# Kernel tuning notes

Hardware: AMD Instinct MI355X
Metric: run time of the kernel (lower is better)

Reference implementation:

```python
import jax, jax.numpy as jnp
import numpy as np

HEAD_DIM = 256
NUM_HEADS = 8
NUM_KV_HEADS = 1
ROPE_BASE = 10000.0
NEG_INF = -1e9


def _rope_cos_sin(position_ids):
    # inv_freq: [head_dim/2]
    inv_freq = 1.0 / (ROPE_BASE ** (jnp.arange(0, HEAD_DIM, 2, dtype=jnp.float32) / HEAD_DIM))
    # freqs: [B, S, head_dim/2]
    freqs = position_ids.astype(jnp.float32)[:, :, None] * inv_freq[None, None, :]
    emb = jnp.concatenate([freqs, freqs], axis=-1)  # [B, S, head_dim]
    return jnp.cos(emb), jnp.sin(emb)


def _rotate_half(x):
    x1, x2 = x[..., : HEAD_DIM // 2], x[..., HEAD_DIM // 2 :]
    return jnp.concatenate([-x2, x1], axis=-1)


def setup_inputs() -> dict:
    key = jax.random.key(0)
    ks = jax.random.split(key, 5)
    B, S, D = 2, 2048, 2048
    hidden_states = jax.random.normal(ks[0], (B, S, D), dtype=jnp.float32)
    # additive causal mask: 0 on/below diagonal, -1e9 above
    causal = jnp.triu(jnp.full((S, S), NEG_INF, dtype=jnp.float32), k=1)
    attention_mask = jnp.broadcast_to(causal[None, None], (B, 1, S, S))
    position_ids = jnp.broadcast_to(jnp.arange(S, dtype=jnp.int64 if jax.config.jax_enable_x64 else jnp.int32)[None], (B, S))
    Wq = jax.random.normal(ks[1], (NUM_HEADS * HEAD_DIM, D), dtype=jnp.float32) * 0.02
    Wk = jax.random.normal(ks[2], (NUM_KV_HEADS * HEAD_DIM, D), dtype=jnp.float32) * 0.02
    Wv = jax.random.normal(ks[3], (NUM_KV_HEADS * HEAD_DIM, D), dtype=jnp.float32) * 0.02
    Wo = jax.random.normal(ks[4], (D, NUM_HEADS * HEAD_DIM), dtype=jnp.float32) * 0.02
    return {"hidden_states": hidden_states, "attention_mask": attention_mask,
            "position_ids": position_ids, "Wq": Wq, "Wk": Wk, "Wv": Wv, "Wo": Wo}


def reference(hidden_states, attention_mask, position_ids, Wq, Wk, Wv, Wo):
    B, S, D = hidden_states.shape
    n_rep = NUM_HEADS // NUM_KV_HEADS
    # projections (no bias)
    q = (hidden_states @ Wq.T).reshape(B, S, NUM_HEADS, HEAD_DIM).transpose(0, 2, 1, 3)
    k = (hidden_states @ Wk.T).reshape(B, S, NUM_KV_HEADS, HEAD_DIM).transpose(0, 2, 1, 3)
    v = (hidden_states @ Wv.T).reshape(B, S, NUM_KV_HEADS, HEAD_DIM).transpose(0, 2, 1, 3)
    # rotary embeddings, broadcast over heads (unsqueeze_dim=1)
    cos, sin = _rope_cos_sin(position_ids)  # [B, S, head_dim]
    cos, sin = cos[:, None], sin[:, None]
    q = q * cos + _rotate_half(q) * sin
    k = k * cos + _rotate_half(k) * sin
    # repeat_kv: expand kv heads to match query heads
    k = jnp.repeat(k, n_rep, axis=1)  # [B, H, S, Dh]
    v = jnp.repeat(v, n_rep, axis=1)
    scores = jnp.einsum('bhqd,bhkd->bhqk', q, k) / jnp.sqrt(jnp.float32(HEAD_DIM))
    scores = scores + attention_mask
    attn_weights = jax.nn.softmax(scores.astype(jnp.float32), axis=-1).astype(q.dtype)
    attn_output = jnp.einsum('bhqk,bhkd->bhqd', attn_weights, v)
    attn_output = attn_output.transpose(0, 2, 1, 3).reshape(B, S, NUM_HEADS * HEAD_DIM)
    attn_output = attn_output @ Wo.T
    return attn_output, attn_weights
```

## Files before the change

### kernel.cpp

```cpp
#include <hip/hip_runtime.h>
#include <math.h>

#define SEQ 2048
#define DM  2048
#define NH  8
#define HD  256
#define NB  2

typedef __attribute__((ext_vector_type(8))) short bf16x8;
typedef __attribute__((ext_vector_type(4))) float f32x4;

__device__ inline short f2b(float f) {
    union { float f; unsigned u; } x; x.f = f;
    unsigned r = x.u + 0x7fffu + ((x.u >> 16) & 1u);
    return (short)(r >> 16);
}
__device__ inline float b2f(short s) {
    union { unsigned u; float f; } x;
    x.u = ((unsigned)(unsigned short)s) << 16;
    return x.f;
}

typedef unsigned int u32_g __attribute__((address_space(1)));
typedef unsigned int u32_l __attribute__((address_space(3)));
__device__ inline void gl2lds(const void* g, void* l) {
    __builtin_amdgcn_global_load_lds((const u32_g*)g, (u32_l*)l, 16, 0, 0);
}

__global__ void convert_all(const float* __restrict__ hs, const float* __restrict__ wq,
                            const float* __restrict__ wk, const float* __restrict__ wv,
                            const float* __restrict__ wo,
                            short* __restrict__ hsb, short* __restrict__ wcat,
                            short* __restrict__ wob)
{
    int i4 = blockIdx.x * 256 + threadIdx.x;
    const float* src; short* dst; int s4, d4;
    if (i4 < 2097152)      { src = hs; dst = hsb;  s4 = i4;           d4 = s4; }
    else if (i4 < 3145728) { src = wq; dst = wcat; s4 = i4 - 2097152; d4 = s4; }
    else if (i4 < 3276800) { src = wk; dst = wcat; s4 = i4 - 3145728; d4 = 1048576 + s4; }
    else if (i4 < 3407872) { src = wv; dst = wcat; s4 = i4 - 3276800; d4 = 1179648 + s4; }
    else                   { src = wo; dst = wob;  s4 = i4 - 3407872; d4 = s4; }
    float4 v = ((const float4*)src)[s4];
    short4 o;
    o.x = f2b(v.x); o.y = f2b(v.y); o.z = f2b(v.z); o.w = f2b(v.w);
    ((short4*)dst)[d4] = o;
}

template<int MODE>
__global__ __launch_bounds__(256, 2) void gemm_bt(const short* __restrict__ A,
                                                  const short* __restrict__ Bw,
                                                  float* __restrict__ C,
                                                  short* __restrict__ q_o,
                                                  short* __restrict__ k_o,
                                                  short* __restrict__ v_o,
                                                  int M, int N, int K)
{
    __shared__ short As[128 * 32];
    __shared__ short Bs[128 * 32];
    int tid = threadIdx.x;
    int lane = tid & 63, w = tid >> 6;
    int lm = lane & 15, quad = lane >> 4;
    int wm = w & 1, wn = w >> 1;
    int m0 = blockIdx.y * 128, n0 = blockIdx.x * 128;

    f32x4 acc[16];
#pragma unroll
    for (int i = 0; i < 16; ++i) acc[i] = (f32x4){0.f, 0.f, 0.f, 0.f};

    const char* Aptr = (const char*)A + (size_t)m0 * K * 2;
    const char* Bptr = (const char*)Bw + (size_t)n0 * K * 2;

    for (int k0 = 0; k0 < K; k0 += 32) {
#pragma unroll
        for (int it = 0; it < 2; ++it) {
            int f = it * 4096 + tid * 16;
            int row = f >> 6, colb = f & 63;
            gl2lds(Aptr + (size_t)row * (K * 2) + k0 * 2 + colb, (char*)As + f);
            gl2lds(Bptr + (size_t)row * (K * 2) + k0 * 2 + colb, (char*)Bs + f);
        }
        __syncthreads();
        bf16x8 af[4], bfr[4];
#pragma unroll
        for (int mt = 0; mt < 4; ++mt)
            af[mt] = *(const bf16x8*)(As + (wm * 64 + mt * 16 + lm) * 32 + quad * 8);
#pragma unroll
        for (int nt = 0; nt < 4; ++nt)
            bfr[nt] = *(const bf16x8*)(Bs + (wn * 64 + nt * 16 + lm) * 32 + quad * 8);
#pragma unroll
        for (int mt = 0; mt < 4; ++mt)
#pragma unroll
            for (int nt = 0; nt < 4; ++nt)
                acc[mt * 4 + nt] = __builtin_amdgcn_mfma_f32_16x16x32_bf16(
                    af[mt], bfr[nt], acc[mt * 4 + nt], 0, 0, 0);
        __syncthreads();
    }

#pragma unroll
    for (int mt = 0; mt < 4; ++mt)
#pragma unroll
        for (int nt = 0; nt < 4; ++nt) {
            f32x4 a = acc[mt * 4 + nt];
            int col = n0 + wn * 64 + nt * 16 + lm;
#pragma unroll
            for (int i = 0; i < 4; ++i) {
                int m = m0 + wm * 64 + mt * 16 + quad * 4 + i;
                if (MODE == 0) {
                    C[(size_t)m * N + col] = a[i];
                } else {
                    int b = m >> 11, s = m & (SEQ - 1);
                    short hv = f2b(a[i]);
                    if (col < DM) {
                        int hh = col >> 8, d = col & (HD - 1);
                        q_o[(((size_t)(b * NH + hh)) * SEQ + s) * HD + d] = hv;
                    } else if (col < DM + HD) {
                        int d = col - DM;
                        int c2 = (d >> 3) ^ (s & 31);
                        k_o[((size_t)b * SEQ + s) * HD + (c2 << 3) + (d & 7)] = hv;
                    } else {
                        int d = col - DM - HD;
                        int sc = ((s >> 3) & 7) ^ (d & 7);
                        v_o[((size_t)(b * HD + d)) * SEQ + (s & ~63) + (sc << 3) + (s & 7)] = hv;
                    }
                }
            }
        }
}

__global__ void rope_kernel(short* __restrict__ q, short* __restrict__ k,
                            const int* __restrict__ pos)
{
    const int QP = NB * NH * SEQ * 128;
    const int KP = NB * SEQ * 128;
    const float C0 = 0.07195578415606394f;
    const float R2PI = 0.15915494309189535f;
    int idx = blockIdx.x * 256 + threadIdx.x;
    if (idx < QP) {
        int d = idx & 127;
        int s = (idx >> 7) & (SEQ - 1);
        int h = (idx >> 18) & (NH - 1);
        int b = idx >> 21;
        float p = (float)pos[b * SEQ + s];
        float fr = p * __expf(-(float)d * C0);
        float rv = fr * R2PI; rv -= floorf(rv);
        float c = __builtin_amdgcn_cosf(rv), sn = __builtin_amdgcn_sinf(rv);
        size_t base = (((size_t)(b * NH + h)) * SEQ + s) * HD + d;
        float x0 = b2f(q[base]), x1 = b2f(q[base + 128]);
        q[base]       = f2b(x0 * c - x1 * sn);
        q[base + 128] = f2b(x1 * c + x0 * sn);
    } else {
        int j = idx - QP;
        if (j < KP) {
            int d = j & 127;
            int s = (j >> 7) & (SEQ - 1);
            int b = j >> 18;
            float p = (float)pos[b * SEQ + s];
            float fr = p * __expf(-(float)d * C0);
            float rv = fr * R2PI; rv -= floorf(rv);
            float c = __builtin_amdgcn_cosf(rv), sn = __builtin_amdgcn_sinf(rv);
            int e0 = ((((d >> 3) ^ (s & 31)) & 31) << 3) | (d & 7);
            size_t base = ((size_t)(b * SEQ + s)) * HD;
            float x0 = b2f(k[base + e0]), x1 = b2f(k[base + (e0 ^ 128)]);
            k[base + e0]         = f2b(x0 * c - x1 * sn);
            k[base + (e0 ^ 128)] = f2b(x1 * c + x0 * sn);
        }
    }
}

__global__ __launch_bounds__(512, 2) void attn_flash(const short* __restrict__ qb,
                                                     const short* __restrict__ kb,
                                                     const short* __restrict__ vT,
                                                     float* __restrict__ w_out,
                                                     short* __restrict__ a_o)
{
    __shared__ short Ks[2][64 * 256];
    __shared__ short Vs[2][256 * 64];
    __shared__ short P[8][16][72];

    const float MCONST = 16.0f;

    int tid = threadIdx.x;
    int w = tid >> 6, lane = tid & 63;
    int lm = lane & 15, quad = lane >> 4;
    int wl = w & 3;
    int grp = w >> 2;
    int idx = blockIdx.x;
    int hb = idx & 15;
    int h = hb & 7, b = hb >> 3;
    int p = idx >> 4;
    int tq = grp ? (31 - p) : p;
    int tmax = 31 - p;
    int q0 = tq * 64;
    int r0 = q0 + wl * 16;

    const short* qrow = qb + (((size_t)(b * NH + h)) * SEQ + r0 + lm) * HD;
    bf16x8 qf[8];
#pragma unroll
    for (int ks = 0; ks < 8; ++ks)
        qf[ks] = *(const bf16x8*)(qrow + ks * 32 + quad * 8);

    float l_r[4];
    f32x4 O[16];
#pragma unroll
    for (int i = 0; i < 4; ++i) l_r[i] = 0.f;
#pragma unroll
    for (int i = 0; i < 16; ++i) O[i] = (f32x4){0.f, 0.f, 0.f, 0.f};

    const short* kb0 = kb + (size_t)b * SEQ * HD;
    const short* vb0 = vT + (size_t)b * HD * SEQ;

    auto STAGE_KV = [&](int t, int bi) {
        const char* kt = (const char*)(kb0 + (size_t)t * 64 * HD);
#pragma unroll
        for (int it = 0; it < 4; ++it) {
            int g = it * 512 + tid;
            gl2lds(kt + ((size_t)(g >> 5) * HD + (g & 31) * 8) * 2, (char*)Ks[bi] + g * 16);
            gl2lds((const char*)vb0 + ((size_t)(g >> 3) * SEQ + t * 64 + (g & 7) * 8) * 2,
                   (char*)Vs[bi] + g * 16);
        }
    };
    auto STAGE_K = [&](int t, int bi) {
        const char* kt = (const char*)(kb0 + (size_t)t * 64 * HD);
#pragma unroll
        for (int it = 0; it < 4; ++it) {
            int g = it * 512 + tid;
            gl2lds(kt + ((size_t)(g >> 5) * HD + (g & 31) * 8) * 2, (char*)Ks[bi] + g * 16);
        }
    };

    STAGE_KV(0, 0);
    asm volatile("s_waitcnt vmcnt(0)" ::: "memory");
    __syncthreads();

    int cur = 0;
    for (int tk = 0; tk <= tmax; ++tk) {
        if (tk < tmax) STAGE_KV(tk + 1, cur ^ 1);

        if (tk <= tq) {
            f32x4 sa[4];
#pragma unroll
            for (int nt = 0; nt < 4; ++nt) sa[nt] = (f32x4){0.f, 0.f, 0.f, 0.f};
            __builtin_amdgcn_s_setprio(1);
#pragma unroll
            for (int ks = 0; ks < 8; ++ks)
#pragma unroll
                for (int nt = 0; nt < 4; ++nt) {
                    int s_l = nt * 16 + lm;
                    bf16x8 kf = *(const bf16x8*)(Ks[cur] + s_l * 256 +
                                                 (((ks * 4 + quad) ^ (s_l & 31)) << 3));
                    sa[nt] = __builtin_amdgcn_mfma_f32_16x16x32_bf16(qf[ks], kf, sa[nt], 0, 0, 0);
                }
            __builtin_amdgcn_s_setprio(0);

#pragma unroll
            for (int nt = 0; nt < 4; ++nt)
#pragma unroll
                for (int i = 0; i < 4; ++i) {
                    float v = sa[nt][i] * 0.0625f;
                    if (tk == tq && (nt * 16 + lm) > (wl * 16 + quad * 4 + i)) v -= 1e9f;
                    float pp = __expf(v - MCONST);
                    l_r[i] += pp;
                    P[w][quad * 4 + i][nt * 16 + lm] = f2b(pp);
                }

            const short* prow = &P[w][lm][0];
            __builtin_amdgcn_s_setprio(1);
#pragma unroll
            for (int kc = 0; kc < 2; ++kc) {
                bf16x8 pf = *(const bf16x8*)(prow + kc * 32 + quad * 8);
#pragma unroll
                for (int nt2 = 0; nt2 < 16; ++nt2) {
                    int d_l = nt2 * 16 + lm;
                    bf16x8 vf = *(const bf16x8*)(Vs[cur] + d_l * 64 +
                                                 (((kc * 4 + quad) ^ (d_l & 7)) << 3));
                    O[nt2] = __builtin_amdgcn_mfma_f32_16x16x32_bf16(pf, vf, O[nt2], 0, 0, 0);
                }
            }
            __builtin_amdgcn_s_setprio(0);
        }

        asm volatile("s_waitcnt vmcnt(0)" ::: "memory");
        __builtin_amdgcn_s_barrier();
        cur ^= 1;
    }

    f32x4 li;
#pragma unroll
    for (int i = 0; i < 4; ++i) {
        float t = l_r[i];
        t += __shfl_xor(t, 1); t += __shfl_xor(t, 2);
        t += __shfl_xor(t, 4); t += __shfl_xor(t, 8);
        li[i] = 1.f / t;
    }

#pragma unroll
    for (int nt2 = 0; nt2 < 16; ++nt2)
#pragma unroll
        for (int i = 0; i < 4; ++i) {
            size_t s = (size_t)q0 + wl * 16 + quad * 4 + i;
            a_o[((size_t)b * SEQ + s) * DM + h * HD + nt2 * 16 + lm] = f2b(O[nt2][i] * li[i]);
        }

    STAGE_K(0, 0);
    asm volatile("s_waitcnt vmcnt(0)" ::: "memory");
    __syncthreads();

    float* wb = w_out + (((size_t)(b * NH + h)) * SEQ) * SEQ;
    cur = 0;
    for (int tk = 0; tk <= tmax; ++tk) {
        if (tk < tmax) STAGE_K(tk + 1, cur ^ 1);

        if (tk <= tq) {
            f32x4 sa[4];
#pragma unroll
            for (int nt = 0; nt < 4; ++nt) sa[nt] = (f32x4){0.f, 0.f, 0.f, 0.f};
            __builtin_amdgcn_s_setprio(1);
#pragma unroll
            for (int ks = 0; ks < 8; ++ks)
#pragma unroll
                for (int nt = 0; nt < 4; ++nt) {
                    int s_l = nt * 16 + lm;
                    bf16x8 kf = *(const bf16x8*)(Ks[cur] + s_l * 256 +
                                                 (((ks * 4 + quad) ^ (s_l & 31)) << 3));
                    sa[nt] = __builtin_amdgcn_mfma_f32_16x16x32_bf16(qf[ks], kf, sa[nt], 0, 0, 0);
                }
            __builtin_amdgcn_s_setprio(0);
#pragma unroll
            for (int nt = 0; nt < 4; ++nt)
#pragma unroll
                for (int i = 0; i < 4; ++i) {
                    float v = sa[nt][i] * 0.0625f;
                    if (tk == tq && (nt * 16 + lm) > (wl * 16 + quad * 4 + i)) v -= 1e9f;
                    float wv = __expf(v - MCONST) * li[i];
                    wb[(size_t)(r0 + quad * 4 + i) * SEQ + tk * 64 + nt * 16 + lm] = wv;
                }
        }

        asm volatile("s_waitcnt vmcnt(0)" ::: "memory");
        __builtin_amdgcn_s_barrier();
        cur ^= 1;
    }

    int zs = (tq + 1) * 64;
    if (zs < SEQ) {
        int tg = tid & 255;
        int r = tg >> 2, c0 = (tg & 3) * 4;
        float* wr = wb + (size_t)(q0 + r) * SEQ;
        f32x4 z = (f32x4){0.f, 0.f, 0.f, 0.f};
        for (int c = zs + c0; c < SEQ; c += 16)
            *(f32x4*)(wr + c) = z;
    }
}

extern "C" void kernel_launch(void* const* d_in, const int* in_sizes, int n_in,
                              void* d_out, int out_size, void* d_ws, size_t ws_size,
                              hipStream_t stream)
{
    const float* hs   = (const float*)d_in[0];
    const int*   pos  = (const int*)d_in[2];
    const float* Wq   = (const float*)d_in[3];
    const float* Wk   = (const float*)d_in[4];
    const float* Wv   = (const float*)d_in[5];
    const float* Wo   = (const float*)d_in[6];

    float* out      = (float*)d_out;
    float* attn_out = out;
    float* w_out    = out + (size_t)NB * SEQ * DM;

    short* hsb  = (short*)d_ws;
    short* a_b  = hsb;
    short* wcat = hsb + 8388608;
    short* wob  = wcat + 5242880;
    short* qx   = wob + 4194304;
    short* kx   = qx + 8388608;
    short* vTx  = kx + 1048576;

    convert_all<<<17408, 256, 0, stream>>>(hs, Wq, Wk, Wv, Wo, hsb, wcat, wob);
    gemm_bt<1><<<dim3(20, 32), 256, 0, stream>>>(hsb, wcat, nullptr, qx, kx, vTx,
                                                 NB * SEQ, DM + 2 * HD, DM);
    rope_kernel<<<18432, 256, 0, stream>>>(qx, kx, pos);
    attn_flash<<<256, 512, 0, stream>>>(qx, kx, vTx, w_out, a_b);
    gemm_bt<0><<<dim3(16, 32), 256, 0, stream>>>(a_b, wob, attn_out, nullptr, nullptr, nullptr,
                                                 NB * SEQ, DM, DM);
}
```

Baseline: 606.9 us.

## Write unnormalized attention weights in flash pass; normalize in separate kernel

Drops the second QK^T recompute pass that regenerated attention weights after the row sums were known. The flash loop now stores the unnormalized exp values straight to the weights output and saves the per-row inverse sums. A new kernel then rescales the causal region and zero-fills the rest. This removes duplicate matmul and K staging work, but the 268MB weights tensor is now read and written once more, which adds a lot of memory traffic.

```diff
diff --git a/kernel.cpp b/kernel.cpp
--- a/kernel.cpp
+++ b/kernel.cpp
@@ -170,7 +170,8 @@
                                                      const short* __restrict__ kb,
                                                      const short* __restrict__ vT,
                                                      float* __restrict__ w_out,
-                                                     short* __restrict__ a_o)
+                                                     short* __restrict__ a_o,
+                                                     float* __restrict__ linv)
 {
     __shared__ short Ks[2][64 * 256];
     __shared__ short Vs[2][256 * 64];
@@ -207,6 +208,7 @@
 
     const short* kb0 = kb + (size_t)b * SEQ * HD;
     const short* vb0 = vT + (size_t)b * HD * SEQ;
+    float* wb = w_out + (((size_t)(b * NH + h)) * SEQ) * SEQ;
 
     auto STAGE_KV = [&](int t, int bi) {
         const char* kt = (const char*)(kb0 + (size_t)t * 64 * HD);
@@ -216,14 +218,6 @@
             gl2lds(kt + ((size_t)(g >> 5) * HD + (g & 31) * 8) * 2, (char*)Ks[bi] + g * 16);
             gl2lds((const char*)vb0 + ((size_t)(g >> 3) * SEQ + t * 64 + (g & 7) * 8) * 2,
                    (char*)Vs[bi] + g * 16);
-        }
-    };
-    auto STAGE_K = [&](int t, int bi) {
-        const char* kt = (const char*)(kb0 + (size_t)t * 64 * HD);
-#pragma unroll
-        for (int it = 0; it < 4; ++it) {
-            int g = it * 512 + tid;
-            gl2lds(kt + ((size_t)(g >> 5) * HD + (g & 31) * 8) * 2, (char*)Ks[bi] + g * 16);
         }
     };
 
@@ -260,6 +254,7 @@
                     float pp = __expf(v - MCONST);
                     l_r[i] += pp;
                     P[w][quad * 4 + i][nt * 16 + lm] = f2b(pp);
+                    wb[(size_t)(r0 + quad * 4 + i) * SEQ + tk * 64 + nt * 16 + lm] = pp;
                 }
 
             const short* prow = &P[w][lm][0];
@@ -290,6 +285,8 @@
         t += __shfl_xor(t, 1); t += __shfl_xor(t, 2);
         t += __shfl_xor(t, 4); t += __shfl_xor(t, 8);
         li[i] = 1.f / t;
+        if (lm == 0)
+            linv[((size_t)(b * NH + h)) * SEQ + r0 + quad * 4 + i] = li[i];
     }
 
 #pragma unroll
@@ -299,55 +296,27 @@
             size_t s = (size_t)q0 + wl * 16 + quad * 4 + i;
             a_o[((size_t)b * SEQ + s) * DM + h * HD + nt2 * 16 + lm] = f2b(O[nt2][i] * li[i]);
         }
-
-    STAGE_K(0, 0);
-    asm volatile("s_waitcnt vmcnt(0)" ::: "memory");
-    __syncthreads();
-
-    float* wb = w_out + (((size_t)(b * NH + h)) * SEQ) * SEQ;
-    cur = 0;
-    for (int tk = 0; tk <= tmax; ++tk) {
-        if (tk < tmax) STAGE_K(tk + 1, cur ^ 1);
-
-        if (tk <= tq) {
-            f32x4 sa[4];
-#pragma unroll
-            for (int nt = 0; nt < 4; ++nt) sa[nt] = (f32x4){0.f, 0.f, 0.f, 0.f};
-            __builtin_amdgcn_s_setprio(1);
-#pragma unroll
-            for (int ks = 0; ks < 8; ++ks)
-#pragma unroll
-                for (int nt = 0; nt < 4; ++nt) {
-                    int s_l = nt * 16 + lm;
-                    bf16x8 kf = *(const bf16x8*)(Ks[cur] + s_l * 256 +
-                                                 (((ks * 4 + quad) ^ (s_l & 31)) << 3));
-                    sa[nt] = __builtin_amdgcn_mfma_f32_16x16x32_bf16(qf[ks], kf, sa[nt], 0, 0, 0);
-                }
-            __builtin_amdgcn_s_setprio(0);
-#pragma unroll
-            for (int nt = 0; nt < 4; ++nt)
-#pragma unroll
-                for (int i = 0; i < 4; ++i) {
-                    float v = sa[nt][i] * 0.0625f;
-                    if (tk == tq && (nt * 16 + lm) > (wl * 16 + quad * 4 + i)) v -= 1e9f;
-                    float wv = __expf(v - MCONST) * li[i];
-                    wb[(size_t)(r0 + quad * 4 + i) * SEQ + tk * 64 + nt * 16 + lm] = wv;
-                }
-        }
-
-        asm volatile("s_waitcnt vmcnt(0)" ::: "memory");
-        __builtin_amdgcn_s_barrier();
-        cur ^= 1;
-    }
-
-    int zs = (tq + 1) * 64;
-    if (zs < SEQ) {
-        int tg = tid & 255;
-        int r = tg >> 2, c0 = (tg & 3) * 4;
-        float* wr = wb + (size_t)(q0 + r) * SEQ;
-        f32x4 z = (f32x4){0.f, 0.f, 0.f, 0.f};
-        for (int c = zs + c0; c < SEQ; c += 16)
-            *(f32x4*)(wr + c) = z;
+}
+
+__global__ __launch_bounds__(256) void normalize_w(float* __restrict__ w,
+                                                   const float* __restrict__ linv)
+{
+    const int CH = NB * NH * SEQ * (SEQ / 4);
+    int tid = blockIdx.x * 256 + threadIdx.x;
+    for (int c = tid; c < CH; c += 2048 * 256) {
+        int row = c >> 9;
+        int c4 = (c & 511) * 4;
+        int s = row & (SEQ - 1);
+        int ks = (s & ~63) + 64;
+        float* p2 = w + (size_t)row * SEQ + c4;
+        if (c4 < ks) {
+            float li = linv[row];
+            f32x4 v = *(const f32x4*)p2;
+            v *= li;
+            *(f32x4*)p2 = v;
+        } else {
+            *(f32x4*)p2 = (f32x4){0.f, 0.f, 0.f, 0.f};
+        }
     }
 }
 
@@ -373,12 +342,14 @@
     short* qx   = wob + 4194304;
     short* kx   = qx + 8388608;
     short* vTx  = kx + 1048576;
+    float* linv = (float*)(vTx + 1048576);
 
     convert_all<<<17408, 256, 0, stream>>>(hs, Wq, Wk, Wv, Wo, hsb, wcat, wob);
     gemm_bt<1><<<dim3(20, 32), 256, 0, stream>>>(hsb, wcat, nullptr, qx, kx, vTx,
                                                  NB * SEQ, DM + 2 * HD, DM);
     rope_kernel<<<18432, 256, 0, stream>>>(qx, kx, pos);
-    attn_flash<<<256, 512, 0, stream>>>(qx, kx, vTx, w_out, a_b);
+    attn_flash<<<256, 512, 0, stream>>>(qx, kx, vTx, w_out, a_b, linv);
     gemm_bt<0><<<dim3(16, 32), 256, 0, stream>>>(a_b, wob, attn_out, nullptr, nullptr, nullptr,
                                                  NB * SEQ, DM, DM);
-}
+    normalize_w<<<2048, 256, 0, stream>>>(w_out, linv);
+}
```

Result: slower. 634.4 us (+4.5%).
